# Kernel optimization log

Hardware: AMD Instinct MI355X
Metric: run time of the kernel (lower is better)

The kernel has to match this reference:

```python
import jax, jax.numpy as jnp
import numpy as np

N_HEADS = 16
R = 256.0


def setup_inputs() -> dict:
    key = jax.random.key(0)
    ks = jax.random.split(key, 8)
    B, T, D, H = 4, 1024, 1024, N_HEADS
    s = 1.0 / np.sqrt(D)
    return {
        "x": jax.random.normal(ks[0], (B, T, D), jnp.float32),
        "Wq": jax.random.normal(ks[1], (D, D), jnp.float32) * s,
        "Wk": jax.random.normal(ks[2], (D, D), jnp.float32) * s,
        "Wv": jax.random.normal(ks[3], (D, D), jnp.float32) * s,
        "Wo": jax.random.normal(ks[4], (D, D), jnp.float32) * s,
        "bo": jnp.zeros((D,), jnp.float32),
        "Wspan": jax.random.normal(ks[5], (H, D), jnp.float32) * s,
        "bspan": jnp.zeros((H,), jnp.float32),
    }


def reference(x, Wq, Wk, Wv, Wo, bo, Wspan, bspan):
    B, T, D = x.shape
    H = N_HEADS
    dh = D // H
    scale = jnp.sqrt(jnp.float32(dh))

    # projections -> (B, H, T, dh)
    def proj(W):
        return jnp.einsum('btd,ed->bte', x, W).reshape(B, T, H, dh).transpose(0, 2, 1, 3)
    Q, K, V = proj(Wq), proj(Wk), proj(Wv)

    # learned span per head: z = T * sigmoid(span_net(mean_t x))  -> (B, H)
    z = T * jax.nn.sigmoid(jnp.einsum('bd,hd->bh', x.mean(axis=1), Wspan) + bspan)

    idx = jnp.arange(T, dtype=jnp.float32)
    dist = idx[None, :] - idx[:, None]          # dist[i,j] = j - i
    causal = dist >= 0                           # matches torch code's mask
    dist_c = jnp.maximum(dist, 0.0)

    scores = jnp.einsum('bhtd,bhsd->bhts', Q, K) / scale
    scores = jnp.where(causal[None, None], scores, -jnp.inf)
    attn = jax.nn.softmax(scores, axis=-1)

    # soft span mask chi_z(h) = clamp((R + z - dist)/R, 0, 1)  (Eq 7)
    span_mask = jnp.clip((R + z[:, :, None, None] - dist_c[None, None]) / R, 0.0, 1.0)
    attn = attn * span_mask
    attn = attn / (attn.sum(axis=-1, keepdims=True) + 1e-8)
    # dropout p=0.0 (eval) -> identity

    out = jnp.einsum('bhts,bhsd->bhtd', attn, V)
    out = out.transpose(0, 2, 1, 3).reshape(B, T, D)
    return jnp.einsum('btd,ed->bte', out, Wo) + bo
```

## Files before the change

kernel.cpp:

```cpp
#include <hip/hip_runtime.h>

#define T_SEQ 1024
#define D_MODEL 1024
#define NH 16
#define DH 64
#define R_SPAN 256.0f

typedef unsigned short ushort_t;
typedef __attribute__((ext_vector_type(8))) short bf16x8;
typedef __attribute__((ext_vector_type(4))) float f32x4;

__device__ __forceinline__ ushort_t f2bf(float f){
  union { float f; unsigned u; } v; v.f = f;
  unsigned r = v.u + 0x7fffu + ((v.u >> 16) & 1u);
  return (ushort_t)(r >> 16);
}

__device__ __forceinline__ float fast_exp2(float x){
#if __has_builtin(__builtin_amdgcn_exp2f)
  return __builtin_amdgcn_exp2f(x);
#else
  return __expf(x * 0.69314718056f);
#endif
}

typedef __attribute__((address_space(1))) void GV;
typedef __attribute__((address_space(3))) void LV;
__device__ __forceinline__ void gld16(const void* g, void* l){
  __builtin_amdgcn_global_load_lds((GV*)g, (LV*)l, 16, 0, 0);
}

__global__ void conv_all(const float* __restrict__ x,
                         const float* s1, const float* s2, const float* s3, const float* s4,
                         ushort_t* __restrict__ x_bf, ushort_t* __restrict__ w_bf){
  const int chunk = blockIdx.y;
  const float* src;
  ushort_t* dst;
  if (chunk < 4){
    src = x + ((size_t)chunk << 20);
    dst = x_bf + ((size_t)chunk << 20);
  } else {
    const float* ws[4] = {s1, s2, s3, s4};
    src = ws[chunk - 4];
    dst = w_bf + ((size_t)(chunk - 4) << 20);
  }
  const int i = (blockIdx.x * 256 + threadIdx.x) * 4;
  float4 v = *(const float4*)(src + i);
  ushort4 o; o.x = f2bf(v.x); o.y = f2bf(v.y); o.z = f2bf(v.z); o.w = f2bf(v.w);
  *(ushort4*)(dst + i) = o;
}

__global__ void mean_kernel(const float* __restrict__ x, float* __restrict__ xmean){
  const int b = blockIdx.y, d0 = blockIdx.x * 64;
  const int dl = threadIdx.x & 63, tg = threadIdx.x >> 6;
  const float* p = x + (size_t)b * T_SEQ * D_MODEL + d0 + dl;
  float s = 0.f;
  for (int t = tg * 256; t < tg * 256 + 256; ++t) s += p[(size_t)t * D_MODEL];
  __shared__ float red[4][64];
  red[tg][dl] = s;
  __syncthreads();
  if (tg == 0){
    float tot = red[0][dl] + red[1][dl] + red[2][dl] + red[3][dl];
    xmean[b * D_MODEL + d0 + dl] = tot * (1.0f / T_SEQ);
  }
}

__global__ void span_kernel(const float* __restrict__ xmean, const float* __restrict__ Wspan,
                            const float* __restrict__ bspan, float* __restrict__ z){
  const int h = blockIdx.x, b = blockIdx.y, l = threadIdx.x;
  const float* xm = xmean + b * D_MODEL;
  const float* wv = Wspan + h * D_MODEL;
  float s = 0.f;
  for (int i = l; i < D_MODEL; i += 64) s += xm[i] * wv[i];
  for (int off = 32; off; off >>= 1) s += __shfl_down(s, off, 64);
  if (l == 0){
    float logit = s + bspan[h];
    z[b * NH + h] = (float)T_SEQ / (1.0f + __expf(-logit));
  }
}

template<int FP32OUT>
__global__ __launch_bounds__(256) void gemm_bt(
    const ushort_t* __restrict__ A,
    const ushort_t* __restrict__ B,
    void* __restrict__ C,
    const float* __restrict__ bias,
    const int M, const int N, const int K)
{
  __shared__ ushort_t At[128 * 32];
  __shared__ ushort_t Bt[128 * 32];

  const int z = blockIdx.z;
  const ushort_t* Bz = B + (size_t)z * N * K;

  const int tid = threadIdx.x;
  const int w = tid >> 6, lane = tid & 63;
  const int q = lane >> 4, c = lane & 15;
  const int m0 = blockIdx.y * 128, n0 = blockIdx.x * 128;
  const int wm = (w >> 1) * 64, wn = (w & 1) * 64;

  const int lr = lane >> 2;
  const int lc = (lane & 3) * 8;

  f32x4 acc[4][4] = {};

  const ushort_t* ga0 = A  + (size_t)(m0 + w * 16 + lr) * K + lc;
  const ushort_t* gb0 = Bz + (size_t)(n0 + w * 16 + lr) * K + lc;

  for (int k0 = 0; k0 < K; k0 += 32){
    __syncthreads();
    gld16(ga0 + k0,              &At[(w * 16) * 32]);
    gld16(ga0 + (size_t)64 * K + k0, &At[(64 + w * 16) * 32]);
    gld16(gb0 + k0,              &Bt[(w * 16) * 32]);
    gld16(gb0 + (size_t)64 * K + k0, &Bt[(64 + w * 16) * 32]);
    __syncthreads();

    bf16x8 af[4], bfv[4];
#pragma unroll
    for (int i = 0; i < 4; ++i) af[i]  = *(const bf16x8*)&At[(wm + i * 16 + c) * 32 + q * 8];
#pragma unroll
    for (int j = 0; j < 4; ++j) bfv[j] = *(const bf16x8*)&Bt[(wn + j * 16 + c) * 32 + q * 8];
#pragma unroll
    for (int i = 0; i < 4; ++i)
#pragma unroll
      for (int j = 0; j < 4; ++j)
        acc[i][j] = __builtin_amdgcn_mfma_f32_16x16x32_bf16(af[i], bfv[j], acc[i][j], 0, 0, 0);
  }

#pragma unroll
  for (int i = 0; i < 4; ++i){
#pragma unroll
    for (int j = 0; j < 4; ++j){
      const int row = m0 + wm + i * 16 + q * 4;
      const int col = n0 + wn + j * 16 + c;
#pragma unroll
      for (int r = 0; r < 4; ++r){
        float v = acc[i][j][r];
        if (FP32OUT){
          ((float*)C)[(size_t)(row + r) * N + col] = v + bias[col];
        } else {
          ((ushort_t*)C + (size_t)z * M * N)[(size_t)(row + r) * N + col] = f2bf(v);
        }
      }
    }
  }
}

#define LP 72
__global__ __launch_bounds__(512) void attn_kernel(
    const ushort_t* __restrict__ Qg,
    const ushort_t* __restrict__ Kg,
    const ushort_t* __restrict__ Vg,
    const float* __restrict__ zspan,
    ushort_t* __restrict__ Og)
{
  __shared__ ushort_t Qs[128 * LP];
  __shared__ ushort_t Ks[64 * LP];
  __shared__ ushort_t Vt[64 * LP];
  __shared__ ushort_t Ps[8][16 * LP];

  const int id = blockIdx.x;
  const int qt = (id >> 3) & 7;
  const int g  = ((id >> 6) << 3) | (id & 7);
  const int b = g >> 4, h = g & 15;
  const int q0 = qt * 128;
  const int tid = threadIdx.x, w = tid >> 6, lane = tid & 63;
  const int q = lane >> 4, c = lane & 15;

  const size_t base = ((size_t)b * T_SEQ) * D_MODEL + (size_t)h * DH;

  {
    const int row = tid >> 2, seg = tid & 3;
    const uint4* gq = (const uint4*)(Qg + base + (size_t)(q0 + row) * D_MODEL);
    uint4* qs = (uint4*)&Qs[row * LP];
    qs[seg * 2]     = gq[seg * 2];
    qs[seg * 2 + 1] = gq[seg * 2 + 1];
  }

  const float zz = zspan[b * NH + h];
  const int jend = min(T_SEQ, (int)(q0 + 127 + R_SPAN + zz) + 1);

  float d0[4] = {0, 0, 0, 0}, d1[4] = {0, 0, 0, 0};
  f32x4 o[4] = {};

  const int wi0 = q0 + w * 16, wi1 = wi0 + 15;
  int i_row[4];
  float ar[4];
#pragma unroll
  for (int r = 0; r < 4; ++r){
    i_row[r] = wi0 + q * 4 + r;
    ar[r] = (R_SPAN + zz + (float)i_row[r]) * (1.0f / R_SPAN);
  }
  const float kexp = 0.125f * 1.44269504f;

  for (int j0 = q0; j0 < jend; j0 += 64){
    __syncthreads();
    {
      const int row = tid >> 3, seg = tid & 7;
      ((uint4*)&Ks[row * LP])[seg] =
          ((const uint4*)(Kg + base + (size_t)(j0 + row) * D_MODEL))[seg];
    }
    {
      const int jrow = tid & 63;
      const int dseg = (tid >> 6) * 8;
      uint4 v = *(const uint4*)(Vg + base + (size_t)(j0 + jrow) * D_MODEL + dseg);
      ushort_t ta[8];
      *(uint4*)ta = v;
#pragma unroll
      for (int i2 = 0; i2 < 8; ++i2) Vt[(dseg + i2) * LP + jrow] = ta[i2];
    }
    __syncthreads();

    if (j0 + 63 < wi0) continue;
    if ((float)(j0 - wi1) > R_SPAN + zz) continue;

    f32x4 s[4] = {};
    {
      bf16x8 aq0 = *(const bf16x8*)&Qs[(w * 16 + c) * LP + q * 8];
      bf16x8 aq1 = *(const bf16x8*)&Qs[(w * 16 + c) * LP + 32 + q * 8];
#pragma unroll
      for (int jf = 0; jf < 4; ++jf){
        bf16x8 bk0 = *(const bf16x8*)&Ks[(jf * 16 + c) * LP + q * 8];
        s[jf] = __builtin_amdgcn_mfma_f32_16x16x32_bf16(aq0, bk0, s[jf], 0, 0, 0);
        bf16x8 bk1 = *(const bf16x8*)&Ks[(jf * 16 + c) * LP + 32 + q * 8];
        s[jf] = __builtin_amdgcn_mfma_f32_16x16x32_bf16(aq1, bk1, s[jf], 0, 0, 0);
      }
    }

    const bool need_mask = (j0 <= wi1);
    const bool full = ((float)(j0 + 63 - wi0) <= zz);

    if (full){
      if (need_mask){
#pragma unroll
        for (int jf = 0; jf < 4; ++jf){
          const int j = j0 + jf * 16 + c;
#pragma unroll
          for (int r = 0; r < 4; ++r){
            float p = fast_exp2(s[jf][r] * kexp);
            p = (j >= i_row[r]) ? p : 0.f;
            d0[r] += p; d1[r] += p;
            Ps[w][(q * 4 + r) * LP + jf * 16 + c] = f2bf(p);
          }
        }
      } else {
#pragma unroll
        for (int jf = 0; jf < 4; ++jf){
#pragma unroll
          for (int r = 0; r < 4; ++r){
            float p = fast_exp2(s[jf][r] * kexp);
            d0[r] += p; d1[r] += p;
            Ps[w][(q * 4 + r) * LP + jf * 16 + c] = f2bf(p);
          }
        }
      }
    } else {
      float fjR[4];
#pragma unroll
      for (int jf = 0; jf < 4; ++jf) fjR[jf] = (float)(j0 + jf * 16 + c) * (1.0f / R_SPAN);
      if (need_mask){
#pragma unroll
        for (int jf = 0; jf < 4; ++jf){
          const int j = j0 + jf * 16 + c;
#pragma unroll
          for (int r = 0; r < 4; ++r){
            float p = fast_exp2(s[jf][r] * kexp);
            p = (j >= i_row[r]) ? p : 0.f;
            float chi = fminf(fmaxf(ar[r] - fjR[jf], 0.f), 1.f);
            float pc = p * chi;
            d0[r] += p; d1[r] += pc;
            Ps[w][(q * 4 + r) * LP + jf * 16 + c] = f2bf(pc);
          }
        }
      } else {
#pragma unroll
        for (int jf = 0; jf < 4; ++jf){
#pragma unroll
          for (int r = 0; r < 4; ++r){
            float p = fast_exp2(s[jf][r] * kexp);
            float chi = fminf(fmaxf(ar[r] - fjR[jf], 0.f), 1.f);
            float pc = p * chi;
            d0[r] += p; d1[r] += pc;
            Ps[w][(q * 4 + r) * LP + jf * 16 + c] = f2bf(pc);
          }
        }
      }
    }

    {
      bf16x8 pa0 = *(const bf16x8*)&Ps[w][c * LP + q * 8];
      bf16x8 pa1 = *(const bf16x8*)&Ps[w][c * LP + 32 + q * 8];
#pragma unroll
      for (int nf = 0; nf < 4; ++nf){
        bf16x8 bv0 = *(const bf16x8*)&Vt[(nf * 16 + c) * LP + q * 8];
        o[nf] = __builtin_amdgcn_mfma_f32_16x16x32_bf16(pa0, bv0, o[nf], 0, 0, 0);
        bf16x8 bv1 = *(const bf16x8*)&Vt[(nf * 16 + c) * LP + 32 + q * 8];
        o[nf] = __builtin_amdgcn_mfma_f32_16x16x32_bf16(pa1, bv1, o[nf], 0, 0, 0);
      }
    }
  }

#pragma unroll
  for (int r = 0; r < 4; ++r){
    float a0 = d0[r], a1 = d1[r];
    a0 += __shfl_xor(a0, 1, 64); a1 += __shfl_xor(a1, 1, 64);
    a0 += __shfl_xor(a0, 2, 64); a1 += __shfl_xor(a1, 2, 64);
    a0 += __shfl_xor(a0, 4, 64); a1 += __shfl_xor(a1, 4, 64);
    a0 += __shfl_xor(a0, 8, 64); a1 += __shfl_xor(a1, 8, 64);
    const float inv = 1.0f / (a1 + 1e-8f * a0);
    const size_t rowbase = base + (size_t)i_row[r] * D_MODEL;
#pragma unroll
    for (int nf = 0; nf < 4; ++nf){
      Og[rowbase + nf * 16 + c] = f2bf(o[nf][r] * inv);
    }
  }
}

extern "C" void kernel_launch(void* const* d_in, const int* in_sizes, int n_in,
                              void* d_out, int out_size, void* d_ws, size_t ws_size,
                              hipStream_t stream)
{
  const float* x     = (const float*)d_in[0];
  const float* Wq    = (const float*)d_in[1];
  const float* Wk    = (const float*)d_in[2];
  const float* Wv    = (const float*)d_in[3];
  const float* Wo    = (const float*)d_in[4];
  const float* bo    = (const float*)d_in[5];
  const float* Wspan = (const float*)d_in[6];
  const float* bspan = (const float*)d_in[7];

  const size_t MT = (size_t)4 * T_SEQ;

  ushort_t* x_bf = (ushort_t*)d_ws;
  ushort_t* w_bf = x_bf + MT * D_MODEL;
  ushort_t* qkv  = w_bf + (size_t)4 * D_MODEL * D_MODEL;
  ushort_t* attn = qkv + (size_t)3 * MT * D_MODEL;
  float* xmean   = (float*)(attn + MT * D_MODEL);
  float* zsp     = xmean + 4 * D_MODEL;

  conv_all<<<dim3(1024, 8), 256, 0, stream>>>(x, Wq, Wk, Wv, Wo, x_bf, w_bf);
  mean_kernel<<<dim3(16, 4), 256, 0, stream>>>(x, xmean);
  span_kernel<<<dim3(16, 4), 64, 0, stream>>>(xmean, Wspan, bspan, zsp);

  gemm_bt<0><<<dim3(8, 32, 3), 256, 0, stream>>>(x_bf, w_bf, qkv, nullptr, 4096, 1024, 1024);

  attn_kernel<<<dim3(512), 512, 0, stream>>>(qkv, qkv + MT * D_MODEL,
                                             qkv + 2 * MT * D_MODEL, zsp, attn);

  gemm_bt<1><<<dim3(8, 32, 1), 256, 0, stream>>>(attn, w_bf + (size_t)3 * D_MODEL * D_MODEL,
                                                 d_out, bo, 4096, 1024, 1024);
}
```

Measured before the change: 206.7 us.

## Double-buffer GEMM tiles, pre-transpose V in projection epilogue, prefetch K/V

The GEMM gains a two-stage LDS double buffer, so the next K-slice load is issued before the current slice's MFMAs and one barrier per iteration goes away. The V projection now writes its output transposed (per batch, feature-major) in packed 4-element stores, which lets the attention kernel load V^T with plain vector copies instead of scattered transposing LDS writes. The attention kernel register-prefetches the next K/V tile while computing on the current one. It also drops the unmasked denominator accumulator and replaces the 1e-8*sum epsilon with a constant, which slightly changes the numerics.

```diff
diff --git a/kernel.cpp b/kernel.cpp
--- a/kernel.cpp
+++ b/kernel.cpp
@@ -87,8 +87,8 @@
     const float* __restrict__ bias,
     const int M, const int N, const int K)
 {
-  __shared__ ushort_t At[128 * 32];
-  __shared__ ushort_t Bt[128 * 32];
+  __shared__ ushort_t At[2][128 * 32];
+  __shared__ ushort_t Bt[2][128 * 32];
 
   const int z = blockIdx.z;
   const ushort_t* Bz = B + (size_t)z * N * K;
@@ -107,19 +107,30 @@
   const ushort_t* ga0 = A  + (size_t)(m0 + w * 16 + lr) * K + lc;
   const ushort_t* gb0 = Bz + (size_t)(n0 + w * 16 + lr) * K + lc;
 
-  for (int k0 = 0; k0 < K; k0 += 32){
+  const int S = K >> 5;
+  gld16(ga0,                   &At[0][(w * 16) * 32]);
+  gld16(ga0 + (size_t)64 * K,  &At[0][(64 + w * 16) * 32]);
+  gld16(gb0,                   &Bt[0][(w * 16) * 32]);
+  gld16(gb0 + (size_t)64 * K,  &Bt[0][(64 + w * 16) * 32]);
+
+  for (int s = 0; s < S; ++s){
     __syncthreads();
-    gld16(ga0 + k0,              &At[(w * 16) * 32]);
-    gld16(ga0 + (size_t)64 * K + k0, &At[(64 + w * 16) * 32]);
-    gld16(gb0 + k0,              &Bt[(w * 16) * 32]);
-    gld16(gb0 + (size_t)64 * K + k0, &Bt[(64 + w * 16) * 32]);
-    __syncthreads();
+    if (s + 1 < S){
+      const int k0 = (s + 1) << 5;
+      const int nb = (s + 1) & 1;
+      gld16(ga0 + k0,                   &At[nb][(w * 16) * 32]);
+      gld16(ga0 + (size_t)64 * K + k0,  &At[nb][(64 + w * 16) * 32]);
+      gld16(gb0 + k0,                   &Bt[nb][(w * 16) * 32]);
+      gld16(gb0 + (size_t)64 * K + k0,  &Bt[nb][(64 + w * 16) * 32]);
+    }
+    const ushort_t* at = At[s & 1];
+    const ushort_t* bt = Bt[s & 1];
 
     bf16x8 af[4], bfv[4];
 #pragma unroll
-    for (int i = 0; i < 4; ++i) af[i]  = *(const bf16x8*)&At[(wm + i * 16 + c) * 32 + q * 8];
-#pragma unroll
-    for (int j = 0; j < 4; ++j) bfv[j] = *(const bf16x8*)&Bt[(wn + j * 16 + c) * 32 + q * 8];
+    for (int i = 0; i < 4; ++i) af[i]  = *(const bf16x8*)&at[(wm + i * 16 + c) * 32 + q * 8];
+#pragma unroll
+    for (int j = 0; j < 4; ++j) bfv[j] = *(const bf16x8*)&bt[(wn + j * 16 + c) * 32 + q * 8];
 #pragma unroll
     for (int i = 0; i < 4; ++i)
 #pragma unroll
@@ -127,20 +138,43 @@
         acc[i][j] = __builtin_amdgcn_mfma_f32_16x16x32_bf16(af[i], bfv[j], acc[i][j], 0, 0, 0);
   }
 
-#pragma unroll
-  for (int i = 0; i < 4; ++i){
-#pragma unroll
-    for (int j = 0; j < 4; ++j){
-      const int row = m0 + wm + i * 16 + q * 4;
-      const int col = n0 + wn + j * 16 + c;
-#pragma unroll
-      for (int r = 0; r < 4; ++r){
-        float v = acc[i][j][r];
-        if (FP32OUT){
-          ((float*)C)[(size_t)(row + r) * N + col] = v + bias[col];
-        } else {
-          ((ushort_t*)C + (size_t)z * M * N)[(size_t)(row + r) * N + col] = f2bf(v);
-        }
+  if (FP32OUT){
+#pragma unroll
+    for (int i = 0; i < 4; ++i){
+#pragma unroll
+      for (int j = 0; j < 4; ++j){
+        const int row = m0 + wm + i * 16 + q * 4;
+        const int col = n0 + wn + j * 16 + c;
+#pragma unroll
+        for (int r = 0; r < 4; ++r)
+          ((float*)C)[(size_t)(row + r) * N + col] = acc[i][j][r] + bias[col];
+      }
+    }
+  } else if (z == 2){
+    ushort_t* Cv = (ushort_t*)C + (size_t)2 * M * N;
+    const int bb = m0 >> 10;
+#pragma unroll
+    for (int i = 0; i < 4; ++i){
+#pragma unroll
+      for (int j = 0; j < 4; ++j){
+        const int col = n0 + wn + j * 16 + c;
+        const int t0 = (m0 & 1023) + wm + i * 16 + q * 4;
+        ushort4 pk;
+        pk.x = f2bf(acc[i][j][0]); pk.y = f2bf(acc[i][j][1]);
+        pk.z = f2bf(acc[i][j][2]); pk.w = f2bf(acc[i][j][3]);
+        *(ushort4*)&Cv[((size_t)bb << 20) + (size_t)col * 1024 + t0] = pk;
+      }
+    }
+  } else {
+#pragma unroll
+    for (int i = 0; i < 4; ++i){
+#pragma unroll
+      for (int j = 0; j < 4; ++j){
+        const int row = m0 + wm + i * 16 + q * 4;
+        const int col = n0 + wn + j * 16 + c;
+#pragma unroll
+        for (int r = 0; r < 4; ++r)
+          ((ushort_t*)C + (size_t)z * M * N)[(size_t)(row + r) * N + col] = f2bf(acc[i][j][r]);
       }
     }
   }
@@ -150,7 +184,7 @@
 __global__ __launch_bounds__(512) void attn_kernel(
     const ushort_t* __restrict__ Qg,
     const ushort_t* __restrict__ Kg,
-    const ushort_t* __restrict__ Vg,
+    const ushort_t* __restrict__ Vtg,
     const float* __restrict__ zspan,
     ushort_t* __restrict__ Og)
 {
@@ -168,6 +202,7 @@
   const int q = lane >> 4, c = lane & 15;
 
   const size_t base = ((size_t)b * T_SEQ) * D_MODEL + (size_t)h * DH;
+  const ushort_t* vtb = Vtg + ((size_t)b << 20) + ((size_t)h << 16);
 
   {
     const int row = tid >> 2, seg = tid & 3;
@@ -180,7 +215,7 @@
   const float zz = zspan[b * NH + h];
   const int jend = min(T_SEQ, (int)(q0 + 127 + R_SPAN + zz) + 1);
 
-  float d0[4] = {0, 0, 0, 0}, d1[4] = {0, 0, 0, 0};
+  float d1[4] = {0, 0, 0, 0};
   f32x4 o[4] = {};
 
   const int wi0 = q0 + w * 16, wi1 = wi0 + 15;
@@ -193,21 +228,20 @@
   }
   const float kexp = 0.125f * 1.44269504f;
 
+  const int srow = tid >> 3, sseg = tid & 7;
+  const ushort_t* kg = Kg + base + sseg * 8;
+  const ushort_t* vg = vtb + (size_t)srow * 1024 + sseg * 8;
+
+  uint4 kreg = *(const uint4*)(kg + (size_t)(q0 + srow) * D_MODEL);
+  uint4 vreg = *(const uint4*)(vg + q0);
+
   for (int j0 = q0; j0 < jend; j0 += 64){
     __syncthreads();
-    {
-      const int row = tid >> 3, seg = tid & 7;
-      ((uint4*)&Ks[row * LP])[seg] =
-          ((const uint4*)(Kg + base + (size_t)(j0 + row) * D_MODEL))[seg];
-    }
-    {
-      const int jrow = tid & 63;
-      const int dseg = (tid >> 6) * 8;
-      uint4 v = *(const uint4*)(Vg + base + (size_t)(j0 + jrow) * D_MODEL + dseg);
-      ushort_t ta[8];
-      *(uint4*)ta = v;
-#pragma unroll
-      for (int i2 = 0; i2 < 8; ++i2) Vt[(dseg + i2) * LP + jrow] = ta[i2];
+    *(uint4*)&Ks[srow * LP + sseg * 8] = kreg;
+    *(uint4*)&Vt[srow * LP + sseg * 8] = vreg;
+    if (j0 + 64 < jend){
+      kreg = *(const uint4*)(kg + (size_t)(j0 + 64 + srow) * D_MODEL);
+      vreg = *(const uint4*)(vg + j0 + 64);
     }
     __syncthreads();
 
@@ -239,7 +273,7 @@
           for (int r = 0; r < 4; ++r){
             float p = fast_exp2(s[jf][r] * kexp);
             p = (j >= i_row[r]) ? p : 0.f;
-            d0[r] += p; d1[r] += p;
+            d1[r] += p;
             Ps[w][(q * 4 + r) * LP + jf * 16 + c] = f2bf(p);
           }
         }
@@ -249,7 +283,7 @@
 #pragma unroll
           for (int r = 0; r < 4; ++r){
             float p = fast_exp2(s[jf][r] * kexp);
-            d0[r] += p; d1[r] += p;
+            d1[r] += p;
             Ps[w][(q * 4 + r) * LP + jf * 16 + c] = f2bf(p);
           }
         }
@@ -268,7 +302,7 @@
             p = (j >= i_row[r]) ? p : 0.f;
             float chi = fminf(fmaxf(ar[r] - fjR[jf], 0.f), 1.f);
             float pc = p * chi;
-            d0[r] += p; d1[r] += pc;
+            d1[r] += pc;
             Ps[w][(q * 4 + r) * LP + jf * 16 + c] = f2bf(pc);
           }
         }
@@ -280,7 +314,7 @@
             float p = fast_exp2(s[jf][r] * kexp);
             float chi = fminf(fmaxf(ar[r] - fjR[jf], 0.f), 1.f);
             float pc = p * chi;
-            d0[r] += p; d1[r] += pc;
+            d1[r] += pc;
             Ps[w][(q * 4 + r) * LP + jf * 16 + c] = f2bf(pc);
           }
         }
@@ -302,12 +336,12 @@
 
 #pragma unroll
   for (int r = 0; r < 4; ++r){
-    float a0 = d0[r], a1 = d1[r];
-    a0 += __shfl_xor(a0, 1, 64); a1 += __shfl_xor(a1, 1, 64);
-    a0 += __shfl_xor(a0, 2, 64); a1 += __shfl_xor(a1, 2, 64);
-    a0 += __shfl_xor(a0, 4, 64); a1 += __shfl_xor(a1, 4, 64);
-    a0 += __shfl_xor(a0, 8, 64); a1 += __shfl_xor(a1, 8, 64);
-    const float inv = 1.0f / (a1 + 1e-8f * a0);
+    float a1 = d1[r];
+    a1 += __shfl_xor(a1, 1, 64);
+    a1 += __shfl_xor(a1, 2, 64);
+    a1 += __shfl_xor(a1, 4, 64);
+    a1 += __shfl_xor(a1, 8, 64);
+    const float inv = 1.0f / (a1 + 1e-20f);
     const size_t rowbase = base + (size_t)i_row[r] * D_MODEL;
 #pragma unroll
     for (int nf = 0; nf < 4; ++nf){
```

Measured after the change: 197.0 us. 4.7% less time.
